# Kernel optimization log

Measured on AMD Instinct MI355X. Metric: run time of the kernel, lower is better.

## Reference

```python
import jax, jax.numpy as jnp
import numpy as np

L_CONST = 10.0   # Lipschitz step size from hyp['L']
LAM = 0.1        # sparsity penalty from hyp['lam']
B, D_IN, D_ENC = 2048, 1024, 4096


def setup_inputs() -> dict:
    key = jax.random.key(0)
    k1, k2 = jax.random.split(key)
    x = jax.random.normal(k1, (B, D_IN, 1), dtype=jnp.float32)
    H = jax.random.normal(k2, (D_IN, D_ENC), dtype=jnp.float32)
    # column-normalize like F.normalize(dim=0)
    H = H / jnp.maximum(jnp.linalg.norm(H, axis=0, keepdims=True), 1e-12)
    return {"x": x, "H": H, "T": 30}


def reference(x, H, T):
    # FISTA sparse coding: T steps of gradient + soft-threshold + Nesterov momentum.
    def step(carry, _):
        x_old, yk, t_old = carry
        r = x - jnp.matmul(H, yk)                      # [B, D_in, 1] residual
        x_new = yk + jnp.matmul(H.T, r) / L_CONST      # [B, D_enc, 1] gradient step
        x_new = jax.nn.relu(jnp.abs(x_new) - LAM / L_CONST) * jnp.sign(x_new)
        t_new = (1.0 + jnp.sqrt(1.0 + 4.0 * t_old * t_old)) / 2.0
        yk_new = x_new + (t_old - 1.0) / t_new * (x_new - x_old)
        return (x_new, yk_new, t_new), None

    zeros = jnp.zeros((x.shape[0], H.shape[1], 1), dtype=x.dtype)
    init = (zeros, zeros, jnp.float32(1.0))
    (x_new, _, _), _ = jax.lax.scan(step, init, None, length=T)
    z = jnp.matmul(H, x_new)                           # [B, D_in, 1] reconstruction
    return z, x_new
```

## Files before the change

### kernel.cpp

```cpp
#include <hip/hip_runtime.h>
#include <hip/hip_bf16.h>
#include <math.h>

#define B_SZ 2048
#define DIN 1024
#define DENC 4096
#define T_ITERS 30

typedef __attribute__((ext_vector_type(8))) short short8;
typedef __attribute__((ext_vector_type(4))) short short4v;
typedef __attribute__((ext_vector_type(4))) float f32x4;

typedef __attribute__((address_space(3))) void lds_void;
typedef const __attribute__((address_space(1))) void glb_void;

__device__ inline short f2bf(float f) {
  union { float f; unsigned u; } v; v.f = f;
  unsigned r = v.u + 0x7fffu + ((v.u >> 16) & 1u);
  return (short)(r >> 16);
}

__device__ inline void gload_lds16(const void* g, void* l) {
  __builtin_amdgcn_global_load_lds((glb_void*)g, (lds_void*)l, 16, 0, 0);
}

template<int N> __device__ inline void waitv() {
  asm volatile("s_waitcnt vmcnt(%0)" :: "n"(N) : "memory");
}

__device__ inline void barrier_raw() {
  asm volatile("" ::: "memory");
  __builtin_amdgcn_s_barrier();
  asm volatile("" ::: "memory");
}

__device__ inline void barrier_nv() {
  asm volatile("s_waitcnt lgkmcnt(0)\n\ts_barrier" ::: "memory");
}

template<int BM, int BN, int K, int MODE, int NBUF>
__global__ __launch_bounds__(256)
void gemm_bt(const short* __restrict__ A, const short* __restrict__ Bm,
             const float* __restrict__ X,
             const float* __restrict__ XC,
             float* __restrict__ XW,
             short* __restrict__ OB,
             float cA, float cB, float cm, int s0, int last, int Nld)
{
  constexpr int WM = BM / 2;
  constexpr int WN = BN / 2;
  constexpr int FM = WM / 16;
  constexpr int FN = WN / 16;
  constexpr int KSTEPS = K / 32;
  constexpr int LPS = (BM + BN) / 64;
  constexpr int BUF_SHORTS = (BM + BN) * 32;
  constexpr int STAGE_SHORTS = NBUF * BUF_SHORTS;
  constexpr int CT_LD = BN + 4;
  constexpr int CT_SHORTS = BM * CT_LD * 2;
  constexpr int SMEM_SHORTS = CT_SHORTS > STAGE_SHORTS ? CT_SHORTS : STAGE_SHORTS;
  constexpr int QITER = (BM * BN) / 1024;

  __shared__ __align__(16) short smem[SMEM_SHORTS];

  const int tid  = threadIdx.x;
  const int lane = tid & 63;
  const int w    = tid >> 6;
  const int wm   = w >> 1, wn = w & 1;
  const long a_row0 = (long)blockIdx.y * BM;
  const long b_row0 = (long)blockIdx.x * BN;

  auto asp = [&](int buf) -> short* { return smem + buf * BUF_SHORTS; };
  auto bsp = [&](int buf) -> short* { return smem + buf * BUF_SHORTS + BM * 32; };

  auto stage = [&](int buf, int kt) {
    const int k0 = kt * 32;
    short* ap = asp(buf);
    short* bp = bsp(buf);
#pragma unroll
    for (int rr = 0; rr < BM / 64; ++rr) {
      int idx16 = rr * 256 + tid;
      int row = idx16 >> 2, ce = (idx16 & 3) * 8;
      gload_lds16(A + (a_row0 + row) * K + k0 + ce,
                  ap + (rr * 256 + (tid & 192)) * 8);
    }
#pragma unroll
    for (int rr = 0; rr < BN / 64; ++rr) {
      int idx16 = rr * 256 + tid;
      int row = idx16 >> 2, ce = (idx16 & 3) * 8;
      gload_lds16(Bm + (b_row0 + row) * K + k0 + ce,
                  bp + (rr * 256 + (tid & 192)) * 8);
    }
  };

  f32x4 acc[FM][FN];
#pragma unroll
  for (int i = 0; i < FM; ++i)
#pragma unroll
    for (int j = 0; j < FN; ++j) acc[i][j] = (f32x4){0.f, 0.f, 0.f, 0.f};

#pragma unroll
  for (int p = 0; p < NBUF - 1; ++p) stage(p, p);

  for (int kt = 0; kt < KSTEPS; ++kt) {
    barrier_raw();
    if (kt + NBUF - 1 < KSTEPS) stage((kt + NBUF - 1) % NBUF, kt + NBUF - 1);
    const int rem = KSTEPS - 1 - kt;
    if constexpr (NBUF >= 4) {
      if (rem >= 3)      waitv<3 * LPS>();
      else if (rem == 2) waitv<2 * LPS>();
      else if (rem == 1) waitv<1 * LPS>();
      else               waitv<0>();
    } else {
      if (rem >= 2)      waitv<2 * LPS>();
      else if (rem == 1) waitv<1 * LPS>();
      else               waitv<0>();
    }
    barrier_raw();

    const short* ap = asp(kt % NBUF);
    const short* bp = bsp(kt % NBUF);
    short8 af[FM], bfr[FN];
#pragma unroll
    for (int i = 0; i < FM; ++i) {
      int row = wm * WM + i * 16 + (lane & 15);
      af[i] = *(const short8*)(ap + row * 32 + (lane >> 4) * 8);
    }
#pragma unroll
    for (int j = 0; j < FN; ++j) {
      int row = wn * WN + j * 16 + (lane & 15);
      bfr[j] = *(const short8*)(bp + row * 32 + (lane >> 4) * 8);
    }
#pragma unroll
    for (int i = 0; i < FM; ++i)
#pragma unroll
      for (int j = 0; j < FN; ++j)
        acc[i][j] = __builtin_amdgcn_mfma_f32_16x16x32_bf16(af[i], bfr[j], acc[i][j], 0, 0, 0);
  }

  f32x4 ld0[QITER], ld1[QITER];
#pragma unroll
  for (int q = 0; q < QITER; ++q) {
    ld0[q] = (f32x4){0.f, 0.f, 0.f, 0.f};
    ld1[q] = (f32x4){0.f, 0.f, 0.f, 0.f};
  }
  if (MODE == 0) {
#pragma unroll
    for (int q = 0; q < QITER; ++q) {
      const int flat = q * 1024 + tid * 4;
      const long gidx = (a_row0 + flat / BN) * (long)Nld + (b_row0 + flat % BN);
      ld0[q] = *(const f32x4*)(X + gidx);
    }
  } else if (MODE == 1) {
    if (!s0) {
#pragma unroll
      for (int q = 0; q < QITER; ++q) {
        const int flat = q * 1024 + tid * 4;
        const long gidx = (a_row0 + flat / BN) * (long)Nld + (b_row0 + flat % BN);
        ld0[q] = *(const f32x4*)(XC + gidx);
        ld1[q] = *(const f32x4*)(XW + gidx);
      }
    }
  }

  barrier_raw();

  float* ct = (float*)smem;
  const int rbase = wm * WM + ((lane >> 4) << 2);
  const int cbase = wn * WN + (lane & 15);
#pragma unroll
  for (int i = 0; i < FM; ++i)
#pragma unroll
    for (int j = 0; j < FN; ++j)
#pragma unroll
      for (int r = 0; r < 4; ++r)
        ct[(rbase + i * 16 + r) * CT_LD + cbase + j * 16] = acc[i][j][r];
  barrier_nv();

  short4v res_ob[QITER];
#pragma unroll
  for (int q = 0; q < QITER; ++q) {
    const int flat = q * 1024 + tid * 4;
    const int row = flat / BN, col = flat % BN;
    const f32x4 cv = *(const f32x4*)(ct + row * CT_LD + col);

    if (MODE == 0) {
      short4v rb;
#pragma unroll
      for (int e = 0; e < 4; ++e) rb[e] = f2bf(ld0[q][e] - cv[e]);
      res_ob[q] = rb;
    } else if (MODE == 2) {
      ld0[q] = cv;
    } else {
      f32x4 xn4; short4v yb;
#pragma unroll
      for (int e = 0; e < 4; ++e) {
        float ykv = cA * ld0[q][e] + cB * ld1[q][e];
        float xg  = ykv + cv[e] * 0.1f;
        float s   = fabsf(xg) - 0.01f;
        float xn  = s > 0.f ? copysignf(s, xg) : 0.f;
        float xo  = ld0[q][e];
        float yn  = xn + cm * (xn - xo);
        xn4[e] = xn;
        yb[e]  = f2bf(last ? xn : yn);
      }
      ld0[q] = xn4;
      res_ob[q] = yb;
    }
  }

#pragma unroll
  for (int q = 0; q < QITER; ++q) {
    const int flat = q * 1024 + tid * 4;
    const long gidx = (a_row0 + flat / BN) * (long)Nld + (b_row0 + flat % BN);
    if (MODE == 0) {
      *(short4v*)(OB + gidx) = res_ob[q];
    } else if (MODE == 2) {
      *(f32x4*)(XW + gidx) = ld0[q];
    } else {
      *(f32x4*)(XW + gidx) = ld0[q];
      *(short4v*)(OB + gidx) = res_ob[q];
    }
  }
}

__global__ void pack_H_kernel(const float* __restrict__ H, short* __restrict__ Hbf,
                              short* __restrict__ Htbf) {
  __shared__ float tile[32][33];
  int tx = threadIdx.x, ty0 = threadIdx.y;
  int j0 = blockIdx.x * 32;
  int i0 = blockIdx.y * 32;
#pragma unroll
  for (int r = 0; r < 4; ++r) {
    int ty = ty0 * 4 + r;
    float v = H[(long)(i0 + ty) * DENC + j0 + tx];
    tile[ty][tx] = v;
    Hbf[(long)(i0 + ty) * DENC + j0 + tx] = f2bf(v);
  }
  __syncthreads();
#pragma unroll
  for (int r = 0; r < 4; ++r) {
    int ty = ty0 * 4 + r;
    Htbf[(long)(j0 + ty) * DIN + i0 + tx] = f2bf(tile[tx][ty]);
  }
}

extern "C" void kernel_launch(void* const* d_in, const int* in_sizes, int n_in,
                              void* d_out, int out_size, void* d_ws, size_t ws_size,
                              hipStream_t stream) {
  const float* x = (const float*)d_in[0];
  const float* H = (const float*)d_in[1];

  float* z_out = (float*)d_out;
  float* xB    = (float*)d_out + (size_t)B_SZ * DIN;

  char* ws = (char*)d_ws;
  size_t off = 0;
  float* xA   = (float*)(ws + off); off += (size_t)B_SZ * DENC * 4;
  short* ykbf = (short*)(ws + off); off += (size_t)B_SZ * DENC * 2;
  short* rbf  = (short*)(ws + off); off += (size_t)B_SZ * DIN  * 2;
  short* Hbf  = (short*)(ws + off); off += (size_t)DIN  * DENC * 2;
  short* Htbf = (short*)(ws + off);

  hipMemsetAsync(ykbf, 0, (size_t)B_SZ * DENC * 2, stream);
  pack_H_kernel<<<dim3(DENC / 32, DIN / 32), dim3(32, 8), 0, stream>>>(H, Hbf, Htbf);

  double t = 1.0, cprev = 0.0;
  for (int s = 0; s < T_ITERS; ++s) {
    gemm_bt<128, 64, DENC, 0, 4><<<dim3(DIN / 64, B_SZ / 128), 256, 0, stream>>>(
        ykbf, Hbf, x, nullptr, nullptr, rbf, 0.f, 0.f, 0.f, 0, 0, DIN);
    double tn = (1.0 + sqrt(1.0 + 4.0 * t * t)) * 0.5;
    float cs = (float)((t - 1.0) / tn);
    const float* xc = (s & 1) ? xA : (const float*)xB;
    float* xw       = (s & 1) ? xB : xA;
    if (s == 0) xc = xB;
    gemm_bt<64, 128, DIN, 1, 3><<<dim3(DENC / 128, B_SZ / 64), 256, 0, stream>>>(
        rbf, Htbf, nullptr, xc, xw, ykbf,
        (float)(1.0 + cprev), (float)(-cprev), cs, (s == 0) ? 1 : 0,
        (s == T_ITERS - 1) ? 1 : 0, DENC);
    cprev = cs; t = tn;
  }
  gemm_bt<128, 64, DENC, 2, 4><<<dim3(DIN / 64, B_SZ / 128), 256, 0, stream>>>(
      ykbf, Hbf, nullptr, nullptr, z_out, nullptr, 0.f, 0.f, 0.f, 0, 0, DIN);
}
```

Measured before the change: 2.523 ms.

## Prefetch epilogue FISTA state before GEMM mainloop and shrink MODE1 tile

For the H^T·r GEMM (MODE 1), the prior x and momentum buffers are now loaded into registers before the K loop, so their global latency overlaps the MFMA mainloop. MODE 0/2 epilogues load X inline per fragment instead of holding all of it in registers, and MODE 1 uses a 64x64 tile with twice as many blocks. The costs are higher register pressure from values held live across the mainloop, and more blocks re-reading the shared operand.

```diff
diff --git a/kernel.cpp b/kernel.cpp
--- a/kernel.cpp
+++ b/kernel.cpp
@@ -59,6 +59,7 @@
   constexpr int CT_SHORTS = BM * CT_LD * 2;
   constexpr int SMEM_SHORTS = CT_SHORTS > STAGE_SHORTS ? CT_SHORTS : STAGE_SHORTS;
   constexpr int QITER = (BM * BN) / 1024;
+  constexpr int EQ = (MODE == 1) ? QITER : 1;
 
   __shared__ __align__(16) short smem[SMEM_SHORTS];
 
@@ -97,6 +98,23 @@
   for (int i = 0; i < FM; ++i)
 #pragma unroll
     for (int j = 0; j < FN; ++j) acc[i][j] = (f32x4){0.f, 0.f, 0.f, 0.f};
+
+  f32x4 ld0[EQ], ld1[EQ];
+#pragma unroll
+  for (int q = 0; q < EQ; ++q) {
+    ld0[q] = (f32x4){0.f, 0.f, 0.f, 0.f};
+    ld1[q] = (f32x4){0.f, 0.f, 0.f, 0.f};
+  }
+  if (MODE == 1 && !s0) {
+#pragma unroll
+    for (int q = 0; q < EQ; ++q) {
+      const int flat = q * 1024 + tid * 4;
+      const long gidx = (a_row0 + flat / BN) * (long)Nld + (b_row0 + flat % BN);
+      ld0[q] = *(const f32x4*)(XC + gidx);
+      ld1[q] = *(const f32x4*)(XW + gidx);
+    }
+    asm volatile("" ::: "memory");
+  }
 
 #pragma unroll
   for (int p = 0; p < NBUF - 1; ++p) stage(p, p);
@@ -137,31 +155,6 @@
         acc[i][j] = __builtin_amdgcn_mfma_f32_16x16x32_bf16(af[i], bfr[j], acc[i][j], 0, 0, 0);
   }
 
-  f32x4 ld0[QITER], ld1[QITER];
-#pragma unroll
-  for (int q = 0; q < QITER; ++q) {
-    ld0[q] = (f32x4){0.f, 0.f, 0.f, 0.f};
-    ld1[q] = (f32x4){0.f, 0.f, 0.f, 0.f};
-  }
-  if (MODE == 0) {
-#pragma unroll
-    for (int q = 0; q < QITER; ++q) {
-      const int flat = q * 1024 + tid * 4;
-      const long gidx = (a_row0 + flat / BN) * (long)Nld + (b_row0 + flat % BN);
-      ld0[q] = *(const f32x4*)(X + gidx);
-    }
-  } else if (MODE == 1) {
-    if (!s0) {
-#pragma unroll
-      for (int q = 0; q < QITER; ++q) {
-        const int flat = q * 1024 + tid * 4;
-        const long gidx = (a_row0 + flat / BN) * (long)Nld + (b_row0 + flat % BN);
-        ld0[q] = *(const f32x4*)(XC + gidx);
-        ld1[q] = *(const f32x4*)(XW + gidx);
-      }
-    }
-  }
-
   barrier_raw();
 
   float* ct = (float*)smem;
@@ -176,21 +169,13 @@
         ct[(rbase + i * 16 + r) * CT_LD + cbase + j * 16] = acc[i][j][r];
   barrier_nv();
 
-  short4v res_ob[QITER];
-#pragma unroll
-  for (int q = 0; q < QITER; ++q) {
-    const int flat = q * 1024 + tid * 4;
-    const int row = flat / BN, col = flat % BN;
-    const f32x4 cv = *(const f32x4*)(ct + row * CT_LD + col);
-
-    if (MODE == 0) {
-      short4v rb;
-#pragma unroll
-      for (int e = 0; e < 4; ++e) rb[e] = f2bf(ld0[q][e] - cv[e]);
-      res_ob[q] = rb;
-    } else if (MODE == 2) {
-      ld0[q] = cv;
-    } else {
+  if constexpr (MODE == 1) {
+    short4v res_ob[QITER];
+    f32x4   res_xn[QITER];
+#pragma unroll
+    for (int q = 0; q < QITER; ++q) {
+      const int flat = q * 1024 + tid * 4;
+      const f32x4 cv = *(const f32x4*)(ct + (flat / BN) * CT_LD + (flat % BN));
       f32x4 xn4; short4v yb;
 #pragma unroll
       for (int e = 0; e < 4; ++e) {
@@ -203,22 +188,32 @@
         xn4[e] = xn;
         yb[e]  = f2bf(last ? xn : yn);
       }
-      ld0[q] = xn4;
+      res_xn[q] = xn4;
       res_ob[q] = yb;
     }
-  }
-
-#pragma unroll
-  for (int q = 0; q < QITER; ++q) {
-    const int flat = q * 1024 + tid * 4;
-    const long gidx = (a_row0 + flat / BN) * (long)Nld + (b_row0 + flat % BN);
-    if (MODE == 0) {
+#pragma unroll
+    for (int q = 0; q < QITER; ++q) {
+      const int flat = q * 1024 + tid * 4;
+      const long gidx = (a_row0 + flat / BN) * (long)Nld + (b_row0 + flat % BN);
+      *(f32x4*)(XW + gidx) = res_xn[q];
       *(short4v*)(OB + gidx) = res_ob[q];
-    } else if (MODE == 2) {
-      *(f32x4*)(XW + gidx) = ld0[q];
-    } else {
-      *(f32x4*)(XW + gidx) = ld0[q];
-      *(short4v*)(OB + gidx) = res_ob[q];
+    }
+  } else {
+#pragma unroll
+    for (int q = 0; q < QITER; ++q) {
+      const int flat = q * 1024 + tid * 4;
+      const int row = flat / BN, col = flat % BN;
+      const f32x4 cv = *(const f32x4*)(ct + row * CT_LD + col);
+      const long gidx = (a_row0 + row) * (long)Nld + (b_row0 + col);
+      if (MODE == 0) {
+        const f32x4 xv = *(const f32x4*)(X + gidx);
+        short4v rb;
+#pragma unroll
+        for (int e = 0; e < 4; ++e) rb[e] = f2bf(xv[e] - cv[e]);
+        *(short4v*)(OB + gidx) = rb;
+      } else {
+        *(f32x4*)(XW + gidx) = cv;
+      }
     }
   }
 }
@@ -273,7 +268,7 @@
     const float* xc = (s & 1) ? xA : (const float*)xB;
     float* xw       = (s & 1) ? xB : xA;
     if (s == 0) xc = xB;
-    gemm_bt<64, 128, DIN, 1, 3><<<dim3(DENC / 128, B_SZ / 64), 256, 0, stream>>>(
+    gemm_bt<64, 64, DIN, 1, 3><<<dim3(DENC / 64, B_SZ / 64), 256, 0, stream>>>(
         rbf, Htbf, nullptr, xc, xw, ykbf,
         (float)(1.0 + cprev), (float)(-cprev), cs, (s == 0) ? 1 : 0,
         (s == T_ITERS - 1) ? 1 : 0, DENC);
```

After: 2.530 ms. About the same (+0.3%).
